# Optimization experiments

Hardware: AMD Instinct MI355X
Metric: run time of the kernel (lower is better)

## Reference

```python
import jax, jax.numpy as jnp
import numpy as np

HEADS = 8
BUCKETS = 64
TEMP = 0.75
SINKHORN_ITER = 5
EPS = 1e-6


def setup_inputs() -> dict:
    key = jax.random.key(0)
    ks = jax.random.split(key, 6)
    b, t, d = 2, 4096, 1024
    x = jax.random.normal(ks[0], (b, t, d), dtype=jnp.float32)
    gumbel_u = jax.random.uniform(ks[1], (b * HEADS, BUCKETS, BUCKETS), dtype=jnp.float32)
    w_qkv = jax.random.normal(ks[2], (d, 3 * d), dtype=jnp.float32) * (d ** -0.5)
    sort_w = jax.random.normal(ks[3], (1, HEADS, (d // HEADS) * 2, BUCKETS), dtype=jnp.float32)
    w_out = jax.random.normal(ks[4], (d, d), dtype=jnp.float32) * (d ** -0.5)
    b_out = jax.random.normal(ks[5], (d,), dtype=jnp.float32) * 0.01
    return {"x": x, "gumbel_u": gumbel_u, "w_qkv": w_qkv, "sort_w": sort_w,
            "w_out": w_out, "b_out": b_out}


def reference(x, gumbel_u, w_qkv, sort_w, w_out, b_out):
    b, t, d = x.shape
    h, buckets = HEADS, BUCKETS
    d_h = d // h
    bsz = t // buckets
    bh = b * h

    # qkv projection (no bias) and head merge -> (b*h, t, d_h)
    qkv = x @ w_qkv
    q, k, v = jnp.split(qkv, 3, axis=2)
    def merge_heads(u):
        return u.reshape(b, t, h, d_h).transpose(0, 2, 1, 3).reshape(bh, t, d_h)
    q, k, v = merge_heads(q), merge_heads(k), merge_heads(v)

    # bucket -> (bh, buckets, bsz, d_h)
    b_q = q.reshape(bh, buckets, bsz, d_h)
    b_k = k.reshape(bh, buckets, bsz, d_h)
    b_v = v.reshape(bh, buckets, bsz, d_h)

    # SortNet: bucket sums -> leaky_relu(x @ W), W per-head (2*d_h, buckets)
    sx = jnp.concatenate([b_q.sum(axis=2), b_k.sum(axis=2)], axis=-1)  # (bh, buckets, 2*d_h)
    W = jnp.broadcast_to(sort_w, (b, h, 2 * d_h, buckets)).reshape(bh, 2 * d_h, buckets)
    R = jax.nn.leaky_relu(jnp.einsum('bue,bec->buc', sx, W), negative_slope=0.01)

    # gumbel-sinkhorn (log clamped for finiteness; matches torch when R >= 0)
    g = -jnp.log(-jnp.log(gumbel_u + EPS) + EPS)
    r = (jnp.log(jnp.maximum(R + EPS, EPS)) + g) / TEMP
    for _ in range(SINKHORN_ITER):
        r = r - jax.nn.logsumexp(r, axis=2, keepdims=True)
        r = r - jax.nn.logsumexp(r, axis=1, keepdims=True)
    R = jnp.exp(r)

    # zero all but top-1 along last dim
    idx = jnp.argmax(R, axis=2)
    R = jnp.where(jnp.arange(buckets)[None, None, :] == idx[..., None], R, 0.0)

    # soft-permute buckets of k and v, concat with locals -> (bh, buckets, 2*bsz, d_h)
    k_r = jnp.einsum('buv,bvtd->butd', R, b_k)
    v_r = jnp.einsum('buv,bvtd->butd', R, b_v)
    b_k2 = jnp.concatenate([k_r, b_k], axis=2)
    b_v2 = jnp.concatenate([v_r, b_v], axis=2)

    # bucketed attention; NOTE: scale uses full model dim d (as in source)
    dots = jnp.einsum('buie,buje->buij', b_q, b_k2) * (d ** -0.5)
    attn = jax.nn.softmax(dots, axis=-1)
    out = jnp.einsum('buij,buje->buie', attn, b_v2)  # (bh, buckets, bsz, d_h)

    out = out.reshape(b, h, t, d_h).transpose(0, 2, 1, 3).reshape(b, t, d)
    return out @ w_out + b_out
```

## Files before the change

kernel.cpp:

```cpp
#include <hip/hip_runtime.h>
#include <stdint.h>

#define TEMP_ 0.75f
#define EPS_ 1e-6f

typedef __attribute__((ext_vector_type(8))) short bf16x8;
typedef __attribute__((ext_vector_type(4))) float f32x4;

typedef __attribute__((address_space(1))) void gvoid_t;
typedef __attribute__((address_space(3))) void lvoid_t;

__device__ __forceinline__ void async_ld16(const void* g, void* l) {
  __builtin_amdgcn_global_load_lds((gvoid_t*)g, (lvoid_t*)l, 16, 0, 0);
}

__device__ __forceinline__ float b2f(ushort u) {
  return __builtin_bit_cast(float, (uint32_t)u << 16);
}
__device__ __forceinline__ ushort f2b(float f) {
  uint32_t x = __builtin_bit_cast(uint32_t, f);
  x += 0x7fffu + ((x >> 16) & 1u);
  return (ushort)(x >> 16);
}

__device__ __forceinline__ uint32_t lds_u32(const void* p) {
  return (uint32_t)(uintptr_t)(lvoid_t*)p;
}

__device__ __forceinline__ bf16x8 dsr(uint32_t addr) {
  bf16x8 d;
  asm volatile("ds_read_b128 %0, %1" : "=v"(d) : "v"(addr));
  return d;
}

__global__ __launch_bounds__(256) void prep_x(
    const float* __restrict__ x, ushort* __restrict__ xb, float* __restrict__ xsum2) {
  const int blk = blockIdx.x;
  const int bu = blk >> 1, half = blk & 1;
  const int b = bu >> 6, u = bu & 63;
  const int c = threadIdx.x * 4;
  const float* src = x + ((size_t)(b * 4096 + u * 64 + half * 32)) * 1024 + c;
  ushort* dst = xb + ((size_t)(b * 4096 + u * 64 + half * 32)) * 1024 + c;
  float s0 = 0.f, s1 = 0.f, s2 = 0.f, s3 = 0.f;
  for (int pos = 0; pos < 32; pos++) {
    float4 v = *(const float4*)(src + (size_t)pos * 1024);
    s0 += v.x; s1 += v.y; s2 += v.z; s3 += v.w;
    ushort4 o;
    o.x = f2b(v.x); o.y = f2b(v.y); o.z = f2b(v.z); o.w = f2b(v.w);
    *(ushort4*)(dst + (size_t)pos * 1024) = o;
  }
  float4 sv = {s0, s1, s2, s3};
  *(float4*)&xsum2[(size_t)blk * 1024 + c] = sv;
}

__global__ __launch_bounds__(256) void transpose_f2b(
    const float* __restrict__ src, ushort* __restrict__ dst, int R, int C) {
  __shared__ float tile[32][33];
  int bx = blockIdx.x * 32;
  int by = blockIdx.y * 32;
  int tx = threadIdx.x & 31, ty = threadIdx.x >> 5;
  #pragma unroll
  for (int i = 0; i < 32; i += 8)
    tile[ty + i][tx] = src[(size_t)(by + ty + i) * C + bx + tx];
  __syncthreads();
  #pragma unroll
  for (int i = 0; i < 32; i += 8)
    dst[(size_t)(bx + ty + i) * R + by + tx] = f2b(tile[tx][ty + i]);
}

__global__ __launch_bounds__(256) void sx_gemm_partial(
    const float* __restrict__ xsum2, const float* __restrict__ wqkv,
    float* __restrict__ SXP) {
  __shared__ float xs[128 * 8];
  const int cb = blockIdx.x;
  const int rt = blockIdx.y;
  const int kc = blockIdx.z;
  const int tid = threadIdx.x;
  for (int idx = tid; idx < 1024; idx += 256) {
    int k = idx >> 3, r = idx & 7;
    int bu = rt * 8 + r;
    int kk = kc * 128 + k;
    xs[idx] = xsum2[(size_t)(bu * 2) * 1024 + kk] + xsum2[(size_t)(bu * 2 + 1) * 1024 + kk];
  }
  __syncthreads();
  const int n = cb * 256 + tid;
  float acc[8];
  #pragma unroll
  for (int r = 0; r < 8; r++) acc[r] = 0.f;
  for (int k = 0; k < 128; k++) {
    float w = wqkv[(size_t)(kc * 128 + k) * 3072 + n];
    float4 a0 = *(const float4*)&xs[k * 8];
    float4 a1 = *(const float4*)&xs[k * 8 + 4];
    acc[0] += a0.x * w; acc[1] += a0.y * w; acc[2] += a0.z * w; acc[3] += a0.w * w;
    acc[4] += a1.x * w; acc[5] += a1.y * w; acc[6] += a1.z * w; acc[7] += a1.w * w;
  }
  #pragma unroll
  for (int r = 0; r < 8; r++)
    SXP[(size_t)(kc * 128 + rt * 8 + r) * 2048 + n] = acc[r];
}

__global__ __launch_bounds__(256) void sx_reduce(
    const float* __restrict__ SXP, float* __restrict__ SX) {
  const int bu = blockIdx.y;
  const int n = blockIdx.x * 256 + threadIdx.x;
  float s = 0.f;
  #pragma unroll
  for (int kc = 0; kc < 8; kc++)
    s += SXP[(size_t)(kc * 128 + bu) * 2048 + n];
  const int head = (n >> 7) & 7;
  const int e2 = ((n >> 10) << 7) | (n & 127);
  const int b = bu >> 6, u = bu & 63;
  SX[((size_t)((b * 8 + head) * 256) + e2) * 64 + u] = s;
}

__global__ __launch_bounds__(256) void sortnet_sinkhorn(
    const float* __restrict__ SX, const float* __restrict__ sortw,
    const float* __restrict__ gum, int* __restrict__ idxArr,
    float* __restrict__ wgtArr) {
  __shared__ float sxl[64 * 64];
  __shared__ float wl[64 * 64];
  __shared__ float rr[64 * 65];
  __shared__ float redA[256];
  __shared__ float redB[256];
  __shared__ int redi[256];
  const int bh = blockIdx.x, tid = threadIdx.x, head = bh & 7;
  const int ui = tid & 15, ci = tid >> 4;

  float acc[4][4];
  #pragma unroll
  for (int i = 0; i < 4; i++)
    #pragma unroll
    for (int j = 0; j < 4; j++) acc[i][j] = 0.f;

  const f32x4* SX4 = (const f32x4*)(SX + (size_t)bh * 16384);
  const f32x4* W4 = (const f32x4*)(sortw + (size_t)head * 16384);
  f32x4* sxl4 = (f32x4*)sxl;
  f32x4* wl4 = (f32x4*)wl;

  #pragma unroll 1
  for (int ch = 0; ch < 4; ch++) {
    __syncthreads();
    #pragma unroll 1
    for (int g = tid; g < 1024; g += 256) {
      sxl4[g] = SX4[ch * 1024 + g];
      wl4[g] = W4[ch * 1024 + g];
    }
    __syncthreads();
    #pragma unroll 2
    for (int e = 0; e < 64; e++) {
      f32x4 a = sxl4[e * 16 + ui];
      f32x4 w = wl4[e * 16 + ci];
      #pragma unroll
      for (int i = 0; i < 4; i++)
        #pragma unroll
        for (int j = 0; j < 4; j++) acc[i][j] += a[i] * w[j];
    }
  }

  #pragma unroll
  for (int i = 0; i < 4; i++)
    #pragma unroll
    for (int j = 0; j < 4; j++) {
      int u = ui * 4 + i, c = ci * 4 + j;
      float dot = acc[i][j];
      float r0 = dot > 0.f ? dot : 0.01f * dot;
      float gu = gum[(size_t)bh * 4096 + u * 64 + c];
      float inner = -logf(gu + EPS_) + EPS_;
      float g = -logf(fmaxf(inner, 1e-38f));
      rr[u * 65 + c] = (logf(fmaxf(r0 + EPS_, EPS_)) + g) / TEMP_;
    }
  __syncthreads();

  const int su = tid & 63, sq = tid >> 6;
  #pragma unroll 1
  for (int it = 0; it < 5; it++) {
    {
      float pm = -1e30f;
      #pragma unroll
      for (int j = 0; j < 16; j++) pm = fmaxf(pm, rr[su * 65 + sq * 16 + j]);
      redA[sq * 64 + su] = pm;
      __syncthreads();
      float m = fmaxf(fmaxf(redA[su], redA[64 + su]), fmaxf(redA[128 + su], redA[192 + su]));
      float ps = 0.f;
      #pragma unroll
      for (int j = 0; j < 16; j++) ps += expf(rr[su * 65 + sq * 16 + j] - m);
      redB[sq * 64 + su] = ps;
      __syncthreads();
      float l = m + logf(redB[su] + redB[64 + su] + redB[128 + su] + redB[192 + su]);
      #pragma unroll
      for (int j = 0; j < 16; j++) rr[su * 65 + sq * 16 + j] -= l;
      __syncthreads();
    }
    {
      float pm = -1e30f;
      #pragma unroll
      for (int j = 0; j < 16; j++) pm = fmaxf(pm, rr[(sq * 16 + j) * 65 + su]);
      redA[sq * 64 + su] = pm;
      __syncthreads();
      float m = fmaxf(fmaxf(redA[su], redA[64 + su]), fmaxf(redA[128 + su], redA[192 + su]));
      float ps = 0.f;
      #pragma unroll
      for (int j = 0; j < 16; j++) ps += expf(rr[(sq * 16 + j) * 65 + su] - m);
      redB[sq * 64 + su] = ps;
      __syncthreads();
      float l = m + logf(redB[su] + redB[64 + su] + redB[128 + su] + redB[192 + su]);
      #pragma unroll
      for (int j = 0; j < 16; j++) rr[(sq * 16 + j) * 65 + su] -= l;
      __syncthreads();
    }
  }

  {
    float pv = -1e30f;
    int pi = 0;
    #pragma unroll
    for (int j = 0; j < 16; j++) {
      float v = rr[su * 65 + sq * 16 + j];
      if (v > pv) { pv = v; pi = sq * 16 + j; }
    }
    redA[sq * 64 + su] = pv;
    redi[sq * 64 + su] = pi;
    __syncthreads();
    if (tid < 64) {
      float best = -1e30f;
      int bi = 0;
      #pragma unroll
      for (int q = 0; q < 4; q++) {
        float v = redA[q * 64 + tid];
        if (v > best) { best = v; bi = redi[q * 64 + tid]; }
      }
      idxArr[bh * 64 + tid] = bi;
      wgtArr[bh * 64 + tid] = expf(fminf(best, 80.f));
    }
  }
}

__global__ __launch_bounds__(256, 2) void gemm_qkv(
    const ushort* __restrict__ A, const ushort* __restrict__ BT,
    ushort* __restrict__ Qb, ushort* __restrict__ Kb, ushort* __restrict__ VT) {
  const int K = 1024;
  __shared__ ushort As[2][128 * 64];
  __shared__ ushort Bs[2][128 * 64];
  const int tid = threadIdx.x;
  const int wave = tid >> 6, lane = tid & 63;
  const int quad = lane >> 4, l16 = lane & 15;
  const int gx = gridDim.x;
  const int lin = blockIdx.y * gx + blockIdx.x;
  const int nwg = gx * gridDim.y;
  const int swz = (lin & 7) * (nwg >> 3) + (lin >> 3);
  const int bx = swz % gx, by = swz / gx;
  const int m0 = by * 128, n0 = bx * 128;
  const int wm = (wave >> 1) * 64, wn = (wave & 1) * 64;
  const ushort* Ap = A + (uint64_t)m0 * K;
  const ushort* Bp = BT + (uint64_t)n0 * K;

  auto stage = [&](const ushort* G, int k0, ushort* buf) {
    #pragma unroll
    for (int q = 0; q < 4; ++q) {
      int p = q * 256 + tid;
      int row = p >> 3, pp = p & 7;
      int cc = pp ^ (row & 7);
      async_ld16(G + (uint64_t)row * K + k0 + cc * 8,
                 buf + (q * 256 + wave * 64) * 8);
    }
  };

  const uint32_t asB = lds_u32(&As[0][0]);
  const uint32_t bsB = lds_u32(&Bs[0][0]);
  uint32_t aoff[2][4], boff[2][4];
  #pragma unroll
  for (int kk = 0; kk < 2; ++kk) {
    int pc = (kk * 4 + quad) ^ (l16 & 7);
    #pragma unroll
    for (int mt = 0; mt < 4; ++mt) {
      aoff[kk][mt] = (uint32_t)((wm + mt * 16 + l16) * 128 + pc * 16);
      boff[kk][mt] = (uint32_t)((wn + mt * 16 + l16) * 128 + pc * 16);
    }
  }

  f32x4 acc[4][4];
  #pragma unroll
  for (int i = 0; i < 4; i++)
    #pragma unroll
    for (int j = 0; j < 4; j++) acc[i][j] = (f32x4){0.f, 0.f, 0.f, 0.f};

  const int NT = K >> 6;
  stage(Ap, 0, As[0]);
  stage(Bp, 0, Bs[0]);
  stage(Ap, 64, As[1]);
  stage(Bp, 64, Bs[1]);

  #pragma unroll 1
  for (int t = 0; t < NT; ++t) {
    if (t < NT - 1)
      asm volatile("s_waitcnt vmcnt(8)\n\ts_barrier" ::: "memory");
    else
      asm volatile("s_waitcnt vmcnt(0)\n\ts_barrier" ::: "memory");

    const uint32_t ab = asB + (uint32_t)(t & 1) * 16384u;
    const uint32_t bb = bsB + (uint32_t)(t & 1) * 16384u;
    bf16x8 a[2][4], b[2][4];
    #pragma unroll
    for (int kk = 0; kk < 2; ++kk) {
      #pragma unroll
      for (int mt = 0; mt < 4; ++mt) a[kk][mt] = dsr(ab + aoff[kk][mt]);
      #pragma unroll
      for (int nt = 0; nt < 4; ++nt) b[kk][nt] = dsr(bb + boff[kk][nt]);
    }
    asm volatile("s_waitcnt lgkmcnt(8)" ::: "memory");
    __builtin_amdgcn_sched_barrier(0);
    __builtin_amdgcn_s_setprio(1);
    #pragma unroll
    for (int mt = 0; mt < 4; ++mt)
      #pragma unroll
      for (int nt = 0; nt < 4; ++nt)
        acc[mt][nt] = __builtin_amdgcn_mfma_f32_16x16x32_bf16(a[0][mt], b[0][nt], acc[mt][nt], 0, 0, 0);
    __builtin_amdgcn_s_setprio(0);
    asm volatile("s_waitcnt lgkmcnt(0)" ::: "memory");
    __builtin_amdgcn_sched_barrier(0);
    __builtin_amdgcn_s_setprio(1);
    #pragma unroll
    for (int mt = 0; mt < 4; ++mt)
      #pragma unroll
      for (int nt = 0; nt < 4; ++nt)
        acc[mt][nt] = __builtin_amdgcn_mfma_f32_16x16x32_bf16(a[1][mt], b[1][nt], acc[mt][nt], 0, 0, 0);
    __builtin_amdgcn_s_setprio(0);
    asm volatile("s_barrier" ::: "memory");
    if (t + 2 < NT) {
      stage(Ap, (t + 2) * 64, As[t & 1]);
      stage(Bp, (t + 2) * 64, Bs[t & 1]);
    }
  }

  int which = bx >> 3;
  int head = bx & 7;
  #pragma unroll
  for (int mt = 0; mt < 4; mt++) {
    int mrow = m0 + wm + mt * 16 + quad * 4;
    int bidx = mrow >> 12;
    int ttok = mrow & 4095;
    int u = ttok >> 6, pos = ttok & 63;
    int bh = bidx * 8 + head;
    #pragma unroll
    for (int nt = 0; nt < 4; nt++) {
      int e = wn + nt * 16 + l16;
      if (which == 2) {
        ushort4 pk;
        pk.x = f2b(acc[mt][nt][0]);
        pk.y = f2b(acc[mt][nt][1]);
        pk.z = f2b(acc[mt][nt][2]);
        pk.w = f2b(acc[mt][nt][3]);
        *(ushort4*)&VT[((uint64_t)(bh * 64 + u) * 128 + e) * 64 + pos] = pk;
      } else {
        ushort* dst = (which == 0) ? Qb : Kb;
        #pragma unroll
        for (int r = 0; r < 4; r++)
          dst[((uint64_t)(bh * 64 + u) * 64 + pos + r) * 128 + e] = f2b(acc[mt][nt][r]);
      }
    }
  }
}

__global__ __launch_bounds__(256, 2) void gemm_out(
    const ushort* __restrict__ A, const ushort* __restrict__ BT,
    int M, int N, int K,
    const float* __restrict__ bias, float* __restrict__ Cout) {
  __shared__ ushort As_lo[128 * 32];
  __shared__ ushort As_hi[128 * 32];
  __shared__ ushort Bs_lo[128 * 32];
  __shared__ ushort Bs_hi[128 * 32];
  const int tid = threadIdx.x;
  const int wave = tid >> 6, lane = tid & 63;
  const int quad = lane >> 4, l16 = lane & 15;
  const int m0 = blockIdx.y * 128, n0 = blockIdx.x * 128;
  const int wm = (wave >> 1) * 64, wn = (wave & 1) * 64;

  f32x4 acc[4][4];
  #pragma unroll
  for (int i = 0; i < 4; i++)
    #pragma unroll
    for (int j = 0; j < 4; j++) acc[i][j] = (f32x4){0.f, 0.f, 0.f, 0.f};

  const int srow = wave * 32 + (lane >> 2);
  const int schunk = (lane & 3) * 8;

  for (int k0 = 0; k0 < K; k0 += 64) {
    __syncthreads();
    {
      const ushort* gA0 = A + (uint64_t)(m0 + srow) * K + k0 + schunk;
      const ushort* gB0 = BT + (uint64_t)(n0 + srow) * K + k0 + schunk;
      const int lofs = (wave * 32) * 32;
      async_ld16(gA0, (ushort*)As_lo + lofs);
      async_ld16(gA0 + (uint64_t)16 * K, (ushort*)As_lo + lofs + 16 * 32);
      async_ld16(gA0 + 32, (ushort*)As_hi + lofs);
      async_ld16(gA0 + (uint64_t)16 * K + 32, (ushort*)As_hi + lofs + 16 * 32);
      async_ld16(gB0, (ushort*)Bs_lo + lofs);
      async_ld16(gB0 + (uint64_t)16 * K, (ushort*)Bs_lo + lofs + 16 * 32);
      async_ld16(gB0 + 32, (ushort*)Bs_hi + lofs);
      async_ld16(gB0 + (uint64_t)16 * K + 32, (ushort*)Bs_hi + lofs + 16 * 32);
    }
    __syncthreads();
    #pragma unroll
    for (int kk = 0; kk < 2; kk++) {
      const ushort* Ab = kk ? As_hi : As_lo;
      const ushort* Bb = kk ? Bs_hi : Bs_lo;
      bf16x8 af[4], bfr[4];
      #pragma unroll
      for (int mt = 0; mt < 4; mt++)
        af[mt] = *(const bf16x8*)&Ab[(wm + mt * 16 + l16) * 32 + quad * 8];
      #pragma unroll
      for (int nt = 0; nt < 4; nt++)
        bfr[nt] = *(const bf16x8*)&Bb[(wn + nt * 16 + l16) * 32 + quad * 8];
      #pragma unroll
      for (int mt = 0; mt < 4; mt++)
        #pragma unroll
        for (int nt = 0; nt < 4; nt++)
          acc[mt][nt] = __builtin_amdgcn_mfma_f32_16x16x32_bf16(af[mt], bfr[nt], acc[mt][nt], 0, 0, 0);
    }
  }

  #pragma unroll
  for (int mt = 0; mt < 4; mt++) {
    int row = m0 + wm + mt * 16 + quad * 4;
    #pragma unroll
    for (int nt = 0; nt < 4; nt++) {
      int col = n0 + wn + nt * 16 + l16;
      float bv = bias[col];
      #pragma unroll
      for (int r = 0; r < 4; r++)
        Cout[(uint64_t)(row + r) * N + col] = acc[mt][nt][r] + bv;
    }
  }
}

#define KSTR 136
__global__ __launch_bounds__(256) void attn_kernel(
    const ushort* __restrict__ Qb, const ushort* __restrict__ Kb,
    const ushort* __restrict__ VT, const int* __restrict__ idxArr,
    const float* __restrict__ wgtArr, ushort* __restrict__ attn_out) {
  __shared__ ushort Qs[64 * KSTR];
  __shared__ ushort Ks[128 * KSTR];
  const int blk = blockIdx.x;
  const int u = blk & 63, bh = blk >> 6;
  const int tid = threadIdx.x, wave = tid >> 6, lane = tid & 63;
  const int quad = lane >> 4, l16 = lane & 15;
  const int vu = idxArr[bh * 64 + u] & 63;
  const float w = wgtArr[bh * 64 + u];

  const ushort* Qsrc = Qb + (uint64_t)(bh * 64 + u) * 8192;
  const ushort* Ksrc0 = Kb + (uint64_t)(bh * 64 + vu) * 8192;
  const ushort* Ksrc1 = Kb + (uint64_t)(bh * 64 + u) * 8192;
  const ushort* Vsrc0 = VT + (uint64_t)(bh * 64 + vu) * 8192;
  const ushort* Vsrc1 = VT + (uint64_t)(bh * 64 + u) * 8192;

  for (int g = tid; g < 64 * 16; g += 256) {
    int eb = g & 15, p = g >> 4;
    *(bf16x8*)&Qs[p * KSTR + eb * 8] = *(const bf16x8*)&Qsrc[p * 128 + eb * 8];
  }
  for (int g = tid; g < 128 * 16; g += 256) {
    int eb = g & 15, j = g >> 4;
    const ushort* s = (j < 64) ? &Ksrc0[j * 128 + eb * 8] : &Ksrc1[(j - 64) * 128 + eb * 8];
    *(bf16x8*)&Ks[j * KSTR + eb * 8] = *(const bf16x8*)s;
  }
  __syncthreads();

  f32x4 S[8];
  #pragma unroll
  for (int nt = 0; nt < 8; nt++) S[nt] = (f32x4){0.f, 0.f, 0.f, 0.f};
  #pragma unroll
  for (int kk = 0; kk < 4; kk++) {
    bf16x8 aq = *(const bf16x8*)&Qs[(wave * 16 + l16) * KSTR + kk * 32 + quad * 8];
    #pragma unroll
    for (int nt = 0; nt < 8; nt++) {
      bf16x8 bk = *(const bf16x8*)&Ks[(nt * 16 + l16) * KSTR + kk * 32 + quad * 8];
      S[nt] = __builtin_amdgcn_mfma_f32_16x16x32_bf16(aq, bk, S[nt], 0, 0, 0);
    }
  }
  __syncthreads();

  for (int g = tid; g < 128 * 16; g += 256) {
    int jb = g & 15, e = g >> 4;
    const ushort* s = (jb < 8) ? &Vsrc0[e * 64 + jb * 8] : &Vsrc1[e * 64 + (jb - 8) * 8];
    *(bf16x8*)&Ks[e * KSTR + jb * 8] = *(const bf16x8*)s;
  }

  const float scale = 0.03125f;
  float rowmax[4] = {-1e30f, -1e30f, -1e30f, -1e30f};
  #pragma unroll
  for (int nt = 0; nt < 8; nt++) {
    float cs = scale * ((nt < 4) ? w : 1.0f);
    #pragma unroll
    for (int r = 0; r < 4; r++) {
      S[nt][r] *= cs;
      rowmax[r] = fmaxf(rowmax[r], S[nt][r]);
    }
  }
  #pragma unroll
  for (int off = 1; off < 16; off <<= 1)
    #pragma unroll
    for (int r = 0; r < 4; r++)
      rowmax[r] = fmaxf(rowmax[r], __shfl_xor(rowmax[r], off, 64));
  float rowsum[4] = {0.f, 0.f, 0.f, 0.f};
  #pragma unroll
  for (int nt = 0; nt < 8; nt++)
    #pragma unroll
    for (int r = 0; r < 4; r++) {
      float p = expf(S[nt][r] - rowmax[r]);
      S[nt][r] = p;
      rowsum[r] += p;
    }
  #pragma unroll
  for (int off = 1; off < 16; off <<= 1)
    #pragma unroll
    for (int r = 0; r < 4; r++)
      rowsum[r] += __shfl_xor(rowsum[r], off, 64);
  float rinv[4];
  #pragma unroll
  for (int r = 0; r < 4; r++) rinv[r] = 1.0f / rowsum[r];

  #pragma unroll
  for (int nt = 0; nt < 8; nt++)
    #pragma unroll
    for (int r = 0; r < 4; r++) {
      float pv = S[nt][r] * rinv[r] * ((nt < 4) ? w : 1.0f);
      Qs[(wave * 16 + quad * 4 + r) * KSTR + nt * 16 + l16] = f2b(pv);
    }
  __syncthreads();

  f32x4 O[8];
  #pragma unroll
  for (int nt = 0; nt < 8; nt++) O[nt] = (f32x4){0.f, 0.f, 0.f, 0.f};
  #pragma unroll
  for (int kk = 0; kk < 4; kk++) {
    bf16x8 ap = *(const bf16x8*)&Qs[(wave * 16 + l16) * KSTR + kk * 32 + quad * 8];
    #pragma unroll
    for (int nt = 0; nt < 8; nt++) {
      bf16x8 bv = *(const bf16x8*)&Ks[(nt * 16 + l16) * KSTR + kk * 32 + quad * 8];
      O[nt] = __builtin_amdgcn_mfma_f32_16x16x32_bf16(ap, bv, O[nt], 0, 0, 0);
    }
  }

  const int bidx = bh >> 3, head = bh & 7;
  uint64_t rowbase =
      (uint64_t)(bidx * 4096 + u * 64 + wave * 16 + quad * 4) * 1024 + head * 128;
  #pragma unroll
  for (int nt = 0; nt < 8; nt++)
    #pragma unroll
    for (int r = 0; r < 4; r++)
      attn_out[rowbase + (uint64_t)r * 1024 + nt * 16 + l16] = f2b(O[nt][r]);
}

extern "C" void kernel_launch(void* const* d_in, const int* in_sizes, int n_in,
                              void* d_out, int out_size, void* d_ws, size_t ws_size,
                              hipStream_t stream) {
  (void)in_sizes; (void)n_in; (void)out_size; (void)ws_size;
  const float* x = (const float*)d_in[0];
  const float* gum = (const float*)d_in[1];
  const float* wqkv = (const float*)d_in[2];
  const float* sortw = (const float*)d_in[3];
  const float* wout = (const float*)d_in[4];
  const float* bout = (const float*)d_in[5];
  float* out = (float*)d_out;

  char* ws = (char*)d_ws;
  size_t off = 0;
  auto alloc = [&](size_t bytes) {
    char* p = ws + off;
    off += (bytes + 255) & ~(size_t)255;
    return p;
  };
  ushort* xb = (ushort*)alloc((size_t)8192 * 1024 * 2);
  float* xsum2 = (float*)alloc((size_t)256 * 1024 * 4);
  ushort* wqkvT = (ushort*)alloc((size_t)3072 * 1024 * 2);
  ushort* woutT = (ushort*)alloc((size_t)1024 * 1024 * 2);
  float* SX = (float*)alloc((size_t)16 * 256 * 64 * 4);
  ushort* Qb = (ushort*)alloc((size_t)16 * 64 * 64 * 128 * 2);
  ushort* Kb = (ushort*)alloc((size_t)16 * 64 * 64 * 128 * 2);
  ushort* VT = (ushort*)alloc((size_t)16 * 64 * 128 * 64 * 2);
  int* idxArr = (int*)alloc((size_t)16 * 64 * 4);
  float* wgtArr = (float*)alloc((size_t)16 * 64 * 4);
  ushort* attn = xb;
  float* SXP = (float*)Qb;

  prep_x<<<256, 256, 0, stream>>>(x, xb, xsum2);
  transpose_f2b<<<dim3(3072 / 32, 1024 / 32), 256, 0, stream>>>(wqkv, wqkvT, 1024, 3072);
  transpose_f2b<<<dim3(1024 / 32, 1024 / 32), 256, 0, stream>>>(wout, woutT, 1024, 1024);
  sx_gemm_partial<<<dim3(8, 16, 8), 256, 0, stream>>>(xsum2, wqkv, SXP);
  sx_reduce<<<dim3(8, 128), 256, 0, stream>>>(SXP, SX);
  sortnet_sinkhorn<<<16, 256, 0, stream>>>(SX, sortw, gum, idxArr, wgtArr);
  gemm_qkv<<<dim3(3072 / 128, 8192 / 128), 256, 0, stream>>>(xb, wqkvT, Qb, Kb, VT);
  attn_kernel<<<16 * 64, 256, 0, stream>>>(Qb, Kb, VT, idxArr, wgtArr, attn);
  gemm_out<<<dim3(1024 / 128, 8192 / 128), 256, 0, stream>>>(
      attn, woutT, 8192, 1024, 1024, bout, out);
}
```

Before: 265.6 us.

## Use quad shuffles in sinkhorn, swizzle out-proj LDS, unroll prep loops

The sinkhorn kernel now gives each row or column to four adjacent lanes and reduces with width-4 shuffles, replacing the shared-memory reduction arrays and two barriers per half-iteration. The output-projection GEMM XOR-swizzles the 16-byte chunk within each LDS row on both the async store side and the ds_read side, to cut bank conflicts. Unroll pragmas are added to the prep_x and sx partial-sum loops. The sinkhorn kernel is small, so the barrier savings may matter little next to the GEMMs.

```diff
diff --git a/kernel.cpp b/kernel.cpp
--- a/kernel.cpp
+++ b/kernel.cpp
@@ -42,6 +42,7 @@
   const float* src = x + ((size_t)(b * 4096 + u * 64 + half * 32)) * 1024 + c;
   ushort* dst = xb + ((size_t)(b * 4096 + u * 64 + half * 32)) * 1024 + c;
   float s0 = 0.f, s1 = 0.f, s2 = 0.f, s3 = 0.f;
+  #pragma unroll 4
   for (int pos = 0; pos < 32; pos++) {
     float4 v = *(const float4*)(src + (size_t)pos * 1024);
     s0 += v.x; s1 += v.y; s2 += v.z; s3 += v.w;
@@ -87,6 +88,7 @@
   float acc[8];
   #pragma unroll
   for (int r = 0; r < 8; r++) acc[r] = 0.f;
+  #pragma unroll 4
   for (int k = 0; k < 128; k++) {
     float w = wqkv[(size_t)(kc * 128 + k) * 3072 + n];
     float4 a0 = *(const float4*)&xs[k * 8];
@@ -120,9 +122,6 @@
   __shared__ float sxl[64 * 64];
   __shared__ float wl[64 * 64];
   __shared__ float rr[64 * 65];
-  __shared__ float redA[256];
-  __shared__ float redB[256];
-  __shared__ int redi[256];
   const int bh = blockIdx.x, tid = threadIdx.x, head = bh & 7;
   const int ui = tid & 15, ci = tid >> 4;
 
@@ -171,41 +170,41 @@
     }
   __syncthreads();
 
-  const int su = tid & 63, sq = tid >> 6;
+  const int row4 = tid >> 2, qq = tid & 3;
   #pragma unroll 1
   for (int it = 0; it < 5; it++) {
     {
       float pm = -1e30f;
       #pragma unroll
-      for (int j = 0; j < 16; j++) pm = fmaxf(pm, rr[su * 65 + sq * 16 + j]);
-      redA[sq * 64 + su] = pm;
-      __syncthreads();
-      float m = fmaxf(fmaxf(redA[su], redA[64 + su]), fmaxf(redA[128 + su], redA[192 + su]));
+      for (int j = 0; j < 16; j++) pm = fmaxf(pm, rr[row4 * 65 + qq * 16 + j]);
+      float m0 = __shfl(pm, 0, 4), m1 = __shfl(pm, 1, 4);
+      float m2 = __shfl(pm, 2, 4), m3 = __shfl(pm, 3, 4);
+      float m = fmaxf(fmaxf(m0, m1), fmaxf(m2, m3));
       float ps = 0.f;
       #pragma unroll
-      for (int j = 0; j < 16; j++) ps += expf(rr[su * 65 + sq * 16 + j] - m);
-      redB[sq * 64 + su] = ps;
-      __syncthreads();
-      float l = m + logf(redB[su] + redB[64 + su] + redB[128 + su] + redB[192 + su]);
-      #pragma unroll
-      for (int j = 0; j < 16; j++) rr[su * 65 + sq * 16 + j] -= l;
+      for (int j = 0; j < 16; j++) ps += expf(rr[row4 * 65 + qq * 16 + j] - m);
+      float s0 = __shfl(ps, 0, 4), s1 = __shfl(ps, 1, 4);
+      float s2 = __shfl(ps, 2, 4), s3 = __shfl(ps, 3, 4);
+      float l = m + logf(((s0 + s1) + s2) + s3);
+      #pragma unroll
+      for (int j = 0; j < 16; j++) rr[row4 * 65 + qq * 16 + j] -= l;
       __syncthreads();
     }
     {
       float pm = -1e30f;
       #pragma unroll
-      for (int j = 0; j < 16; j++) pm = fmaxf(pm, rr[(sq * 16 + j) * 65 + su]);
-      redA[sq * 64 + su] = pm;
-      __syncthreads();
-      float m = fmaxf(fmaxf(redA[su], redA[64 + su]), fmaxf(redA[128 + su], redA[192 + su]));
+      for (int j = 0; j < 16; j++) pm = fmaxf(pm, rr[(qq * 16 + j) * 65 + row4]);
+      float m0 = __shfl(pm, 0, 4), m1 = __shfl(pm, 1, 4);
+      float m2 = __shfl(pm, 2, 4), m3 = __shfl(pm, 3, 4);
+      float m = fmaxf(fmaxf(m0, m1), fmaxf(m2, m3));
       float ps = 0.f;
       #pragma unroll
-      for (int j = 0; j < 16; j++) ps += expf(rr[(sq * 16 + j) * 65 + su] - m);
-      redB[sq * 64 + su] = ps;
-      __syncthreads();
-      float l = m + logf(redB[su] + redB[64 + su] + redB[128 + su] + redB[192 + su]);
-      #pragma unroll
-      for (int j = 0; j < 16; j++) rr[(sq * 16 + j) * 65 + su] -= l;
+      for (int j = 0; j < 16; j++) ps += expf(rr[(qq * 16 + j) * 65 + row4] - m);
+      float s0 = __shfl(ps, 0, 4), s1 = __shfl(ps, 1, 4);
+      float s2 = __shfl(ps, 2, 4), s3 = __shfl(ps, 3, 4);
+      float l = m + logf(((s0 + s1) + s2) + s3);
+      #pragma unroll
+      for (int j = 0; j < 16; j++) rr[(qq * 16 + j) * 65 + row4] -= l;
       __syncthreads();
     }
   }
@@ -215,22 +214,22 @@
     int pi = 0;
     #pragma unroll
     for (int j = 0; j < 16; j++) {
-      float v = rr[su * 65 + sq * 16 + j];
-      if (v > pv) { pv = v; pi = sq * 16 + j; }
-    }
-    redA[sq * 64 + su] = pv;
-    redi[sq * 64 + su] = pi;
-    __syncthreads();
-    if (tid < 64) {
-      float best = -1e30f;
-      int bi = 0;
-      #pragma unroll
-      for (int q = 0; q < 4; q++) {
-        float v = redA[q * 64 + tid];
-        if (v > best) { best = v; bi = redi[q * 64 + tid]; }
-      }
-      idxArr[bh * 64 + tid] = bi;
-      wgtArr[bh * 64 + tid] = expf(fminf(best, 80.f));
+      float v = rr[row4 * 65 + qq * 16 + j];
+      if (v > pv) { pv = v; pi = qq * 16 + j; }
+    }
+    float v0 = __shfl(pv, 0, 4); int i0 = __shfl(pi, 0, 4);
+    float v1 = __shfl(pv, 1, 4); int i1 = __shfl(pi, 1, 4);
+    float v2 = __shfl(pv, 2, 4); int i2 = __shfl(pi, 2, 4);
+    float v3 = __shfl(pv, 3, 4); int i3 = __shfl(pi, 3, 4);
+    float best = -1e30f;
+    int bi = 0;
+    if (v0 > best) { best = v0; bi = i0; }
+    if (v1 > best) { best = v1; bi = i1; }
+    if (v2 > best) { best = v2; bi = i2; }
+    if (v3 > best) { best = v3; bi = i3; }
+    if (qq == 0) {
+      idxArr[bh * 64 + row4] = bi;
+      wgtArr[bh * 64 + row4] = expf(fminf(best, 80.f));
     }
   }
 }
@@ -382,7 +381,8 @@
     for (int j = 0; j < 4; j++) acc[i][j] = (f32x4){0.f, 0.f, 0.f, 0.f};
 
   const int srow = wave * 32 + (lane >> 2);
-  const int schunk = (lane & 3) * 8;
+  const int schunk = ((lane & 3) ^ ((srow >> 1) & 3)) * 8;
+  const int qsw = (quad ^ ((l16 >> 1) & 3)) * 8;
 
   for (int k0 = 0; k0 < K; k0 += 64) {
     __syncthreads();
@@ -407,10 +407,10 @@
       bf16x8 af[4], bfr[4];
       #pragma unroll
       for (int mt = 0; mt < 4; mt++)
-        af[mt] = *(const bf16x8*)&Ab[(wm + mt * 16 + l16) * 32 + quad * 8];
+        af[mt] = *(const bf16x8*)&Ab[(wm + mt * 16 + l16) * 32 + qsw];
       #pragma unroll
       for (int nt = 0; nt < 4; nt++)
-        bfr[nt] = *(const bf16x8*)&Bb[(wn + nt * 16 + l16) * 32 + quad * 8];
+        bfr[nt] = *(const bf16x8*)&Bb[(wn + nt * 16 + l16) * 32 + qsw];
       #pragma unroll
       for (int mt = 0; mt < 4; mt++)
         #pragma unroll
```

Result: no change. 262.3 us (-1.2%).
